# Kernel optimization log

Measured on AMD Instinct MI355X. Metric: run time of the kernel, lower is better.

Reference implementation:

```python
import jax, jax.numpy as jnp
import numpy as np

TEMPERATURE = 0.1
B, S, D, V = 4, 256, 768, 50257


def setup_inputs() -> dict:
    key = jax.random.key(0)
    k1, k2 = jax.random.split(key)
    return {
        "pred_embeds": jax.random.normal(k1, (B, S, D), dtype=jnp.float32),
        "embed_weight": jax.random.normal(k2, (V, D), dtype=jnp.float32),
    }


def reference(pred_embeds, embed_weight):
    # metric == 'l2': scores = -||p - t||^2, computed via the GEMM identity
    # -(||p||^2 + ||t||^2 - 2 p.t) instead of a (B,S,V,D) broadcast diff.
    p_sq = jnp.sum(pred_embeds * pred_embeds, axis=-1)        # (B,S)
    t_sq = jnp.sum(embed_weight * embed_weight, axis=-1)      # (V,)
    dot = jnp.einsum('bsd,vd->bsv', pred_embeds, embed_weight)  # (B,S,V)
    scores = 2.0 * dot - p_sq[..., None] - t_sq               # (B,S,V)

    softmax_pred_probs = jax.nn.softmax(scores / TEMPERATURE, axis=-1)
    predictions = jnp.argmax(softmax_pred_probs, axis=-1)      # (B,S) int

    # straight-through one-hot over probs
    y_hard = jax.nn.one_hot(predictions, V, dtype=softmax_pred_probs.dtype)
    pred_probs = y_hard - jax.lax.stop_gradient(softmax_pred_probs) + softmax_pred_probs

    # straight-through embedding lookup
    n_pred_embs = embed_weight[predictions]                    # (B,S,D)
    pred_embeds_st = pred_embeds + jax.lax.stop_gradient(n_pred_embs - pred_embeds)

    return (pred_embeds_st, pred_embeds, predictions, pred_probs, softmax_pred_probs)
```

## Files before the change

### kernel.cpp

```cpp
#include <hip/hip_runtime.h>
#include <math.h>

namespace {

constexpr int Bb = 4, Ss = 256, Dd = 768, Vv = 50257;
constexpr int Mm = Bb * Ss;
constexpr int BM = 128, BN = 128, BK = 32;
constexpr int NS = Dd / BK;
constexpr int TW = (Vv + BN - 1) / BN;
constexpr int TA = Mm / BM;
constexpr int CHUNK = BM * BK;
constexpr float SC = 14.4269504088896341f;

typedef _Float16 f16x8 __attribute__((ext_vector_type(8)));
typedef float f32x4 __attribute__((ext_vector_type(4)));

constexpr size_t WPLANE = (size_t)TW * NS * CHUNK;
constexpr size_t APLANE = (size_t)TA * NS * CHUNK;

__device__ __forceinline__ void gload_lds16(const void* g, void* l) {
    typedef __attribute__((address_space(3))) void lds_t;
    typedef const __attribute__((address_space(1))) void gm_t;
    __builtin_amdgcn_global_load_lds((gm_t*)g, (lds_t*)l, 16, 0, 0);
}

__global__ __launch_bounds__(256) void convert_pack_tsq(const float* __restrict__ src,
                                                        _Float16* __restrict__ hp,
                                                        _Float16* __restrict__ lp,
                                                        float* __restrict__ sumsq,
                                                        int nrows) {
    const int t   = blockIdx.x;
    const int tid = threadIdx.x;
    const int r   = blockIdx.y * 64 + (tid >> 2);
    const int q   = tid & 3;
    const int v   = t * BM + r;
    const bool valid = v < nrows;

    float sq = 0.f;
#pragma unroll
    for (int i = 0; i < 6; ++i) {
        const int s = q * 6 + i;
        float vals[32];
        if (valid) {
            const float4* p = reinterpret_cast<const float4*>(src + (size_t)v * Dd + s * BK);
#pragma unroll
            for (int k = 0; k < 8; ++k) *reinterpret_cast<float4*>(&vals[4 * k]) = p[k];
        } else {
#pragma unroll
            for (int k = 0; k < 32; ++k) vals[k] = 0.f;
        }
        const size_t chunk = ((size_t)t * NS + s) * CHUNK;
#pragma unroll
        for (int fq = 0; fq < 4; ++fq) {
            _Float16 hi[8], lo[8];
#pragma unroll
            for (int e = 0; e < 8; ++e) {
                const float x = vals[fq * 8 + e];
                sq = fmaf(x, x, sq);
                const _Float16 h = (_Float16)x;
                hi[e] = h;
                lo[e] = (_Float16)(x - (float)h);
            }
            *reinterpret_cast<f16x8*>(&hp[chunk + fq * (BM * 8) + (size_t)r * 8]) =
                *reinterpret_cast<const f16x8*>(hi);
            *reinterpret_cast<f16x8*>(&lp[chunk + fq * (BM * 8) + (size_t)r * 8]) =
                *reinterpret_cast<const f16x8*>(lo);
        }
    }
    sq += __shfl_xor(sq, 1);
    sq += __shfl_xor(sq, 2);
    if (valid && q == 0) sumsq[v] = sq;
}

__global__ __launch_bounds__(256) void gemm_kernel(const _Float16* __restrict__ Ahp,
                                                   const _Float16* __restrict__ Alp,
                                                   const _Float16* __restrict__ Whp,
                                                   const _Float16* __restrict__ Wlp,
                                                   const float* __restrict__ tsq,
                                                   float* __restrict__ scores) {
    __shared__ _Float16 lds[4][CHUNK];

    const int b    = blockIdx.x;
    const int xcd  = b & 7;
    const int slot = b >> 3;
    const int tn   = xcd * 50 + (slot >> 3);
    const int tm   = slot & 7;
    if (tn >= TW) return;

    const int tid  = threadIdx.x;
    const int wid  = tid >> 6;
    const int lane = tid & 63;
    const int wr   = wid >> 1;
    const int wc   = wid & 1;
    const int fr   = lane & 15;
    const int fq   = lane >> 4;

    const _Float16* gA_h = Ahp + (size_t)tm * NS * CHUNK;
    const _Float16* gA_l = Alp + (size_t)tm * NS * CHUNK;
    const _Float16* gW_h = Whp + (size_t)tn * NS * CHUNK;
    const _Float16* gW_l = Wlp + (size_t)tn * NS * CHUNK;

    f32x4 acc[4][4];
#pragma unroll
    for (int m = 0; m < 4; ++m)
#pragma unroll
        for (int n = 0; n < 4; ++n) acc[m][n] = (f32x4){0.f, 0.f, 0.f, 0.f};

    for (int s = 0; s < NS; ++s) {
        if (s) __syncthreads();
        const size_t so = (size_t)s * CHUNK;
        const _Float16* gsrc[4] = {gA_h + so, gA_l + so, gW_h + so, gW_l + so};
#pragma unroll
        for (int c = 0; c < 4; ++c) {
#pragma unroll
            for (int i = 0; i < 2; ++i) {
                const int seg = wid * 2 + i;
                gload_lds16(gsrc[c] + seg * 512 + lane * 8, &lds[c][seg * 512]);
            }
        }
        __syncthreads();

        f16x8 ah[4], al[4];
#pragma unroll
        for (int m = 0; m < 4; ++m) {
            const int r = wr * 64 + m * 16 + fr;
            ah[m] = *reinterpret_cast<const f16x8*>(&lds[0][fq * (BM * 8) + r * 8]);
            al[m] = *reinterpret_cast<const f16x8*>(&lds[1][fq * (BM * 8) + r * 8]);
        }
#pragma unroll
        for (int n = 0; n < 4; ++n) {
            const int c = wc * 64 + n * 16 + fr;
            const f16x8 wh = *reinterpret_cast<const f16x8*>(&lds[2][fq * (BM * 8) + c * 8]);
            const f16x8 wl = *reinterpret_cast<const f16x8*>(&lds[3][fq * (BM * 8) + c * 8]);
#pragma unroll
            for (int m = 0; m < 4; ++m) {
                acc[m][n] = __builtin_amdgcn_mfma_f32_16x16x32_f16(ah[m], wh, acc[m][n], 0, 0, 0);
                acc[m][n] = __builtin_amdgcn_mfma_f32_16x16x32_f16(al[m], wh, acc[m][n], 0, 0, 0);
                acc[m][n] = __builtin_amdgcn_mfma_f32_16x16x32_f16(ah[m], wl, acc[m][n], 0, 0, 0);
            }
        }
    }

#pragma unroll
    for (int n = 0; n < 4; ++n) {
        const int gn = tn * BN + wc * 64 + n * 16 + fr;
        if (gn >= Vv) continue;
        const float t = tsq[gn];
#pragma unroll
        for (int m = 0; m < 4; ++m) {
            const int gm = tm * BM + wr * 64 + m * 16 + fq * 4;
#pragma unroll
            for (int r = 0; r < 4; ++r) {
                scores[(size_t)(gm + r) * Vv + gn] = fmaf(2.f, acc[m][n][r], -t);
            }
        }
    }
}

__global__ __launch_bounds__(256) void finalize_kernel(const float* __restrict__ A,
                                                       const float* __restrict__ W,
                                                       float* __restrict__ out0,
                                                       float* __restrict__ out1,
                                                       float* __restrict__ out2,
                                                       float* __restrict__ out3,
                                                       float* __restrict__ out4) {
    const int row = blockIdx.x;
    const int tid = threadIdx.x;
    float* srow = out4 + (size_t)row * Vv;
    float* hrow = out3 + (size_t)row * Vv;
    constexpr int NV4 = Vv >> 2;

    const float4* s4 = reinterpret_cast<const float4*>(srow);

    float m4[4]  = {-INFINITY, -INFINITY, -INFINITY, -INFINITY};
    int   id4[4] = {0, 0, 0, 0};
    float sm4[4] = {0.f, 0.f, 0.f, 0.f};
    for (int i = tid; i < NV4; i += 256) {
        const float4 v = s4[i];
        const float vv[4] = {v.x, v.y, v.z, v.w};
#pragma unroll
        for (int j = 0; j < 4; ++j) {
            const float val = vv[j];
            if (val > m4[j]) {
                sm4[j] *= exp2f((m4[j] - val) * SC);
                m4[j] = val;
                id4[j] = 4 * i + j;
            }
            sm4[j] += exp2f((val - m4[j]) * SC);
        }
    }
    float m = m4[0];
    int   idx = id4[0];
    float sum = sm4[0];
#pragma unroll
    for (int j = 1; j < 4; ++j) {
        if (m4[j] > m || (m4[j] == m && id4[j] < idx)) {
            sum = sum * exp2f((m - m4[j]) * SC) + sm4[j];
            m = m4[j];
            idx = id4[j];
        } else {
            sum += sm4[j] * exp2f((m4[j] - m) * SC);
        }
    }
    if (tid == 0) {
        const float val = srow[Vv - 1];
        if (val > m) { sum *= exp2f((m - val) * SC); m = val; idx = Vv - 1; }
        sum += exp2f((val - m) * SC);
    }

    __shared__ float smax[256];
    __shared__ int   sidx[256];
    __shared__ float ssum[256];
    smax[tid] = m; sidx[tid] = idx; ssum[tid] = sum;
    __syncthreads();
#pragma unroll
    for (int off = 128; off > 0; off >>= 1) {
        if (tid < off) {
            const float m1 = smax[tid], m2 = smax[tid + off];
            const int   i1 = sidx[tid], i2 = sidx[tid + off];
            const float s1 = ssum[tid], s2 = ssum[tid + off];
            if (m2 > m1 || (m2 == m1 && i2 < i1)) {
                smax[tid] = m2; sidx[tid] = i2;
                ssum[tid] = s1 * exp2f((m1 - m2) * SC) + s2;
            } else {
                ssum[tid] = s1 + s2 * exp2f((m2 - m1) * SC);
            }
        }
        __syncthreads();
    }
    const float gmax = smax[0];
    const int   pred = sidx[0];
    const float inv  = 1.0f / ssum[0];
    __syncthreads();

    float4* p4 = reinterpret_cast<float4*>(srow);
    float4* h4 = reinterpret_cast<float4*>(hrow);
    for (int i = tid; i < NV4; i += 256) {
        const float4 v = s4[i];
        const int b = 4 * i;
        float4 p, h;
        p.x = exp2f((v.x - gmax) * SC) * inv;
        p.y = exp2f((v.y - gmax) * SC) * inv;
        p.z = exp2f((v.z - gmax) * SC) * inv;
        p.w = exp2f((v.w - gmax) * SC) * inv;
        h.x = (b + 0 == pred) ? 1.f : 0.f;
        h.y = (b + 1 == pred) ? 1.f : 0.f;
        h.z = (b + 2 == pred) ? 1.f : 0.f;
        h.w = (b + 3 == pred) ? 1.f : 0.f;
        p4[i] = p;
        h4[i] = h;
    }
    if (tid == 0) {
        const float val = srow[Vv - 1];
        srow[Vv - 1] = exp2f((val - gmax) * SC) * inv;
        hrow[Vv - 1] = (pred == Vv - 1) ? 1.f : 0.f;
        out2[row] = (float)pred;
    }

    const float4* wrow = reinterpret_cast<const float4*>(W + (size_t)pred * Dd);
    const float4* arow = reinterpret_cast<const float4*>(A + (size_t)row * Dd);
    float4* o0 = reinterpret_cast<float4*>(out0 + (size_t)row * Dd);
    float4* o1 = reinterpret_cast<float4*>(out1 + (size_t)row * Dd);
    if (tid < Dd / 4) {
        o0[tid] = wrow[tid];
        o1[tid] = arow[tid];
    }
}

}

extern "C" void kernel_launch(void* const* d_in, const int* in_sizes, int n_in,
                              void* d_out, int out_size, void* d_ws, size_t ws_size,
                              hipStream_t stream) {
    const float* pred_embeds  = (const float*)d_in[0];
    const float* embed_weight = (const float*)d_in[1];

    float* out  = (float*)d_out;
    float* out0 = out;
    float* out1 = out0 + (size_t)Mm * Dd;
    float* out2 = out1 + (size_t)Mm * Dd;
    float* out3 = out2 + Mm;
    float* out4 = out3 + (size_t)Mm * Vv;

    _Float16* Whp = (_Float16*)out3;
    _Float16* Wlp = Whp + WPLANE;
    _Float16* Ahp = Wlp + WPLANE;
    _Float16* Alp = Ahp + APLANE;
    float*    tsq = (float*)(Alp + APLANE);
    float*    asq = tsq + Vv;

    convert_pack_tsq<<<dim3(TW, 2), 256, 0, stream>>>(embed_weight, Whp, Wlp, tsq, Vv);
    convert_pack_tsq<<<dim3(TA, 2), 256, 0, stream>>>(pred_embeds, Ahp, Alp, asq, Mm);

    gemm_kernel<<<3200, 256, 0, stream>>>(Ahp, Alp, Whp, Wlp, tsq, out4);

    finalize_kernel<<<Mm, 256, 0, stream>>>(pred_embeds, embed_weight,
                                            out0, out1, out2, out3, out4);
}
```

Baseline: 519.0 us.

## Fuse per-tile softmax max/argmax/sum partials into GEMM epilogue with reduce kernel

The GEMM epilogue now computes per-row, per-64-column partial max, argmax and rescaled exp-sum, and writes them to a workspace. A new reduce_stats kernel combines these partials per row and stashes the max, inverse sum and prediction in spare output slots. The finalize kernel no longer needs its first full pass over the 50257-wide score row. This removes one full read of the large scores matrix, in exchange for extra epilogue shuffles and exp work in the GEMM plus one more kernel launch.

Result: slower. 628.2 us (+21.0%).

```diff
diff --git a/kernel.cpp b/kernel.cpp
--- a/kernel.cpp
+++ b/kernel.cpp
@@ -9,6 +9,7 @@
 constexpr int NS = Dd / BK;
 constexpr int TW = (Vv + BN - 1) / BN;
 constexpr int TA = Mm / BM;
+constexpr int NT2 = TW * 2;
 constexpr int CHUNK = BM * BK;
 constexpr float SC = 14.4269504088896341f;
 
@@ -77,7 +78,10 @@
                                                    const _Float16* __restrict__ Whp,
                                                    const _Float16* __restrict__ Wlp,
                                                    const float* __restrict__ tsq,
-                                                   float* __restrict__ scores) {
+                                                   float* __restrict__ scores,
+                                                   float* __restrict__ pmax,
+                                                   int*   __restrict__ pidx,
+                                                   float* __restrict__ psum) {
     __shared__ _Float16 lds[4][CHUNK];
 
     const int b    = blockIdx.x;
@@ -154,6 +158,99 @@
                 scores[(size_t)(gm + r) * Vv + gn] = fmaf(2.f, acc[m][n][r], -t);
             }
         }
+    }
+
+    const int cidx = tn * 2 + wc;
+#pragma unroll
+    for (int m = 0; m < 4; ++m) {
+#pragma unroll
+        for (int r = 0; r < 4; ++r) {
+            const int grow = tm * BM + wr * 64 + m * 16 + fq * 4 + r;
+            float vals[4];
+            float vmax = -INFINITY;
+            int   vidx = 0x7fffffff;
+#pragma unroll
+            for (int n = 0; n < 4; ++n) {
+                const int gn = tn * BN + wc * 64 + n * 16 + fr;
+                const bool ok = gn < Vv;
+                const float t = ok ? tsq[gn] : 0.f;
+                const float sv = ok ? fmaf(2.f, acc[m][n][r], -t) : -INFINITY;
+                vals[n] = sv;
+                if (sv > vmax) { vmax = sv; vidx = gn; }
+            }
+            float lsum = 0.f;
+#pragma unroll
+            for (int n = 0; n < 4; ++n)
+                if (vals[n] > -INFINITY) lsum += exp2f((vals[n] - vmax) * SC);
+
+            float wm = vmax; int wi = vidx;
+#pragma unroll
+            for (int off = 1; off < 16; off <<= 1) {
+                const float om = __shfl_xor(wm, off);
+                const int   oi = __shfl_xor(wi, off);
+                if (om > wm || (om == wm && oi < wi)) { wm = om; wi = oi; }
+            }
+            float rs = (vmax > -INFINITY) ? lsum * exp2f((vmax - wm) * SC) : 0.f;
+#pragma unroll
+            for (int off = 1; off < 16; off <<= 1) rs += __shfl_xor(rs, off);
+
+            if (fr == 0) {
+                const size_t o = (size_t)grow * NT2 + cidx;
+                pmax[o] = wm;
+                pidx[o] = wi;
+                psum[o] = rs;
+            }
+        }
+    }
+}
+
+__global__ __launch_bounds__(256) void reduce_stats(const float* __restrict__ pmax,
+                                                    const int*   __restrict__ pidx,
+                                                    const float* __restrict__ psum,
+                                                    float* __restrict__ out1,
+                                                    float* __restrict__ out2) {
+    const int row = blockIdx.x;
+    const int tid = threadIdx.x;
+    const size_t base = (size_t)row * NT2;
+
+    float m = -INFINITY, s = 0.f;
+    int   id = 0x7fffffff;
+    for (int c = tid; c < NT2; c += 256) {
+        const float m2 = pmax[base + c];
+        const int   i2 = pidx[base + c];
+        const float s2 = psum[base + c];
+        if (m2 > m || (m2 == m && i2 < id)) {
+            s = ((m > -INFINITY) ? s * exp2f((m - m2) * SC) : 0.f) + s2;
+            m = m2; id = i2;
+        } else {
+            s += (m2 > -INFINITY) ? s2 * exp2f((m2 - m) * SC) : 0.f;
+        }
+    }
+
+    __shared__ float smax[256];
+    __shared__ int   sidx[256];
+    __shared__ float ssum[256];
+    smax[tid] = m; sidx[tid] = id; ssum[tid] = s;
+    __syncthreads();
+#pragma unroll
+    for (int off = 128; off > 0; off >>= 1) {
+        if (tid < off) {
+            const float m1 = smax[tid], m2 = smax[tid + off];
+            const int   i1 = sidx[tid], i2 = sidx[tid + off];
+            const float s1 = ssum[tid], s2 = ssum[tid + off];
+            if (m2 > m1 || (m2 == m1 && i2 < i1)) {
+                smax[tid] = m2; sidx[tid] = i2;
+                ssum[tid] = ((m1 > -INFINITY) ? s1 * exp2f((m1 - m2) * SC) : 0.f) + s2;
+            } else {
+                ssum[tid] = s1 + ((m2 > -INFINITY) ? s2 * exp2f((m2 - m1) * SC) : 0.f);
+            }
+        }
+        __syncthreads();
+    }
+    if (tid == 0) {
+        out2[row] = (float)sidx[0];
+        out1[(size_t)row * Dd + 766] = smax[0];
+        out1[(size_t)row * Dd + 767] = 1.0f / ssum[0];
     }
 }
 
@@ -170,69 +267,11 @@
     float* hrow = out3 + (size_t)row * Vv;
     constexpr int NV4 = Vv >> 2;
 
+    const float gmax = out1[(size_t)row * Dd + 766];
+    const float inv  = out1[(size_t)row * Dd + 767];
+    const int   pred = (int)out2[row];
+
     const float4* s4 = reinterpret_cast<const float4*>(srow);
-
-    float m4[4]  = {-INFINITY, -INFINITY, -INFINITY, -INFINITY};
-    int   id4[4] = {0, 0, 0, 0};
-    float sm4[4] = {0.f, 0.f, 0.f, 0.f};
-    for (int i = tid; i < NV4; i += 256) {
-        const float4 v = s4[i];
-        const float vv[4] = {v.x, v.y, v.z, v.w};
-#pragma unroll
-        for (int j = 0; j < 4; ++j) {
-            const float val = vv[j];
-            if (val > m4[j]) {
-                sm4[j] *= exp2f((m4[j] - val) * SC);
-                m4[j] = val;
-                id4[j] = 4 * i + j;
-            }
-            sm4[j] += exp2f((val - m4[j]) * SC);
-        }
-    }
-    float m = m4[0];
-    int   idx = id4[0];
-    float sum = sm4[0];
-#pragma unroll
-    for (int j = 1; j < 4; ++j) {
-        if (m4[j] > m || (m4[j] == m && id4[j] < idx)) {
-            sum = sum * exp2f((m - m4[j]) * SC) + sm4[j];
-            m = m4[j];
-            idx = id4[j];
-        } else {
-            sum += sm4[j] * exp2f((m4[j] - m) * SC);
-        }
-    }
-    if (tid == 0) {
-        const float val = srow[Vv - 1];
-        if (val > m) { sum *= exp2f((m - val) * SC); m = val; idx = Vv - 1; }
-        sum += exp2f((val - m) * SC);
-    }
-
-    __shared__ float smax[256];
-    __shared__ int   sidx[256];
-    __shared__ float ssum[256];
-    smax[tid] = m; sidx[tid] = idx; ssum[tid] = sum;
-    __syncthreads();
-#pragma unroll
-    for (int off = 128; off > 0; off >>= 1) {
-        if (tid < off) {
-            const float m1 = smax[tid], m2 = smax[tid + off];
-            const int   i1 = sidx[tid], i2 = sidx[tid + off];
-            const float s1 = ssum[tid], s2 = ssum[tid + off];
-            if (m2 > m1 || (m2 == m1 && i2 < i1)) {
-                smax[tid] = m2; sidx[tid] = i2;
-                ssum[tid] = s1 * exp2f((m1 - m2) * SC) + s2;
-            } else {
-                ssum[tid] = s1 + s2 * exp2f((m2 - m1) * SC);
-            }
-        }
-        __syncthreads();
-    }
-    const float gmax = smax[0];
-    const int   pred = sidx[0];
-    const float inv  = 1.0f / ssum[0];
-    __syncthreads();
-
     float4* p4 = reinterpret_cast<float4*>(srow);
     float4* h4 = reinterpret_cast<float4*>(hrow);
     for (int i = tid; i < NV4; i += 256) {
@@ -254,8 +293,9 @@
         const float val = srow[Vv - 1];
         srow[Vv - 1] = exp2f((val - gmax) * SC) * inv;
         hrow[Vv - 1] = (pred == Vv - 1) ? 1.f : 0.f;
-        out2[row] = (float)pred;
-    }
+    }
+
+    __syncthreads();
 
     const float4* wrow = reinterpret_cast<const float4*>(W + (size_t)pred * Dd);
     const float4* arow = reinterpret_cast<const float4*>(A + (size_t)row * Dd);
@@ -288,11 +328,17 @@
     _Float16* Alp = Ahp + APLANE;
     float*    tsq = (float*)(Alp + APLANE);
     float*    asq = tsq + Vv;
+    float*    pmax = asq + Mm;
+    int*      pidx = (int*)(pmax + (size_t)Mm * NT2);
+    float*    psum = (float*)(pidx + (size_t)Mm * NT2);
 
     convert_pack_tsq<<<dim3(TW, 2), 256, 0, stream>>>(embed_weight, Whp, Wlp, tsq, Vv);
     convert_pack_tsq<<<dim3(TA, 2), 256, 0, stream>>>(pred_embeds, Ahp, Alp, asq, Mm);
 
-    gemm_kernel<<<3200, 256, 0, stream>>>(Ahp, Alp, Whp, Wlp, tsq, out4);
+    gemm_kernel<<<3200, 256, 0, stream>>>(Ahp, Alp, Whp, Wlp, tsq, out4,
+                                          pmax, pidx, psum);
+
+    reduce_stats<<<Mm, 256, 0, stream>>>(pmax, pidx, psum, out1, out2);
 
     finalize_kernel<<<Mm, 256, 0, stream>>>(pred_embeds, embed_weight,
                                             out0, out1, out2, out3, out4);
```
